# Kernel optimization log

Hardware: AMD Instinct MI355X
Metric: run time of the kernel (lower is better)

The kernel has to match this reference:

```python
import jax, jax.numpy as jnp
import numpy as np

L = 4096   # num_tokens (one prefill sequence)
D = 2048   # hidden_size
HK = 16    # num_k_heads
HV = 32    # num_v_heads
DK = 128   # head_k_dim
DV = 128   # head_v_dim
RATIO = HV // HK
EPS = 1e-6


def setup_inputs() -> dict:
    key = jax.random.key(0)
    ks = jax.random.split(key, 11)
    s = 0.02
    return {
        "hidden_states": jax.random.normal(ks[0], (L, D), jnp.float32),
        "Wq": jax.random.normal(ks[1], (D, HK * DK), jnp.float32) * s,
        "Wk": jax.random.normal(ks[2], (D, HK * DK), jnp.float32) * s,
        "Wv": jax.random.normal(ks[3], (D, HV * DV), jnp.float32) * s,
        "Wz": jax.random.normal(ks[4], (D, HV * DV), jnp.float32) * s,
        "Wb": jax.random.normal(ks[5], (D, HV), jnp.float32) * s,
        "Wa": jax.random.normal(ks[6], (D, HV), jnp.float32) * s,
        "A_log": jnp.log(jax.random.uniform(ks[7], (HV,), jnp.float32, 1.0, 16.0)),
        "dt_bias": jax.random.normal(ks[8], (HV,), jnp.float32) * 0.5,
        "norm_weight": jnp.ones((DV,), jnp.float32),
        "W_out": jax.random.normal(ks[9], (HV * DV, D), jnp.float32) * s,
    }


def _l2norm(x):
    return x * jax.lax.rsqrt(jnp.sum(x * x, axis=-1, keepdims=True) + EPS)


def reference(hidden_states, Wq, Wk, Wv, Wz, Wb, Wa, A_log, dt_bias, norm_weight, W_out):
    h = hidden_states
    # --- input projections (qkvz + ba split) ---
    q = _l2norm((h @ Wq).reshape(L, HK, DK))            # [L, HK, DK]
    k = _l2norm((h @ Wk).reshape(L, HK, DK))
    v = (h @ Wv).reshape(L, HV, DV)                     # [L, HV, DV]
    z = (h @ Wz).reshape(L, HV, DV)                     # gate for RMSNorm
    beta = jax.nn.sigmoid(h @ Wb)                       # [L, HV]
    g = -jnp.exp(A_log) * jax.nn.softplus(h @ Wa + dt_bias)  # [L, HV]
    decay = jnp.exp(g)                                  # per-token per-head decay
    # repeat shared q/k heads to value heads (GQA ratio)
    q = jnp.repeat(q, RATIO, axis=1) * (DK ** -0.5)     # [L, HV, DK]
    k = jnp.repeat(k, RATIO, axis=1)

    # --- gated delta rule recurrence over tokens ---
    def step(S, xs):
        q_t, k_t, v_t, b_t, d_t = xs                    # [HV,DK],[HV,DK],[HV,DV],[HV],[HV]
        S = S * d_t[:, None, None]                      # decay state [HV, DK, DV]
        pred = jnp.einsum('hk,hkv->hv', k_t, S)         # memory readout
        delta = (v_t - pred) * b_t[:, None]             # delta-rule correction
        S = S + k_t[:, :, None] * delta[:, None, :]
        o = jnp.einsum('hk,hkv->hv', q_t, S)
        return S, o

    S0 = jnp.zeros((HV, DK, DV), jnp.float32)
    _, core = jax.lax.scan(step, S0, (q, k, v, beta, decay))  # core: [L, HV, DV]

    # --- gated RMSNorm: x * silu(z), rms-normalize over head dim ---
    x = core * jax.nn.silu(z)
    x = x * jax.lax.rsqrt(jnp.mean(x * x, axis=-1, keepdims=True) + EPS) * norm_weight

    # --- output projection ---
    return x.reshape(L, HV * DV) @ W_out                # [L, D]
```

## Files before the change

### kernel.cpp

```cpp
#include <hip/hip_runtime.h>

#define LTOK 4096
#define DHID 2048
#define HKN  16
#define HVN  32
#define DKK  128
#define NTOT 12288

typedef unsigned short u16;
typedef __attribute__((ext_vector_type(8))) short short8;
typedef __attribute__((ext_vector_type(8))) unsigned short u16x8;
typedef __attribute__((ext_vector_type(4))) unsigned short u16x4;
typedef __attribute__((ext_vector_type(4))) float f32x4;

__device__ __forceinline__ float b2f(u16 u) {
  unsigned int x = ((unsigned int)u) << 16;
  return __builtin_bit_cast(float, x);
}
__device__ __forceinline__ u16 f2bf(float f) {
  unsigned int u = __builtin_bit_cast(unsigned int, f);
  u += 0x7FFFu + ((u >> 16) & 1u);
  return (u16)(u >> 16);
}

template<int C> __device__ __forceinline__ float dppmv(float x) {
  int i = __builtin_amdgcn_update_dpp(0, __builtin_bit_cast(int, x), C, 0xF, 0xF, true);
  return __builtin_bit_cast(float, i);
}
__device__ __forceinline__ float red16(float x) {
  x += dppmv<0xB1>(x);
  x += dppmv<0x4E>(x);
  x += dppmv<0x124>(x);
  x += dppmv<0x128>(x);
  return x;
}

__device__ __forceinline__ void gld16(const void* g, void* l) {
  __builtin_amdgcn_global_load_lds((const __attribute__((address_space(1))) void*)g,
                                   (__attribute__((address_space(3))) void*)l, 16, 0, 0);
}

template<int OFF> __device__ __forceinline__ short8 dsr(unsigned a) {
  short8 r;
  asm volatile("ds_read_b128 %0, %1 offset:%2" : "=v"(r) : "v"(a), "n"(OFF));
  return r;
}

__device__ __forceinline__ int sw16(int r, int c, int rowc) { return (r * rowc + c) ^ ((r & 7) << 3); }

__device__ __forceinline__ void cstore(u16* C, size_t i, float v) { C[i] = f2bf(v); }
__device__ __forceinline__ void cstore(float* C, size_t i, float v) { C[i] = v; }

__global__ __launch_bounds__(256)
void k_cvt(const float* __restrict__ s, u16* __restrict__ d, int n) {
  const int i = (blockIdx.x * 256 + threadIdx.x) * 4;
  const float4 v = *(const float4*)(s + i);
  ushort4 o;
  o.x = f2bf(v.x); o.y = f2bf(v.y); o.z = f2bf(v.z); o.w = f2bf(v.w);
  *(ushort4*)(d + i) = o;
}

__global__ __launch_bounds__(256)
void k_tr(const float* __restrict__ src, u16* __restrict__ dst, int R, int C) {
  __shared__ float tl[32][33];
  const int r0 = blockIdx.y * 32, c0 = blockIdx.x * 32;
  const int tr = threadIdx.x >> 3, tc = (threadIdx.x & 7) * 4;
  const float4 v = *(const float4*)(src + (size_t)(r0 + tr) * C + c0 + tc);
  tl[tr][tc] = v.x; tl[tr][tc + 1] = v.y; tl[tr][tc + 2] = v.z; tl[tr][tc + 3] = v.w;
  __syncthreads();
  ushort4 o;
  o.x = f2bf(tl[tc + 0][tr]); o.y = f2bf(tl[tc + 1][tr]);
  o.z = f2bf(tl[tc + 2][tr]); o.w = f2bf(tl[tc + 3][tr]);
  *(ushort4*)(dst + (size_t)(c0 + tr) * R + r0 + tc) = o;
}

#define MFMA16(a, b, c) __builtin_amdgcn_mfma_f32_16x16x32_bf16(a, b, c, 0, 0, 0)

template<typename OutT, int NWN>
__global__ __launch_bounds__(512, 2)
void k_g256(const u16* __restrict__ A, const u16* __restrict__ Bt, OutT* __restrict__ C,
            int M, int N, int K, int NT) {
  constexpr int BUFE = 8192 + NWN * 2048;
  constexpr int BN = NWN * 64;
  __shared__ u16 Lds[4 * BUFE];
  const int tid = threadIdx.x;
  const int lane = tid & 63, w = tid >> 6;
  const int fr = lane & 15, fq = lane >> 4;
  const int wm = (w >> 2) * 128, wn = (w & 3) * (NWN * 16);
  const int nkt = K >> 5;
  const size_t sK = (size_t)K;

  const int MT = gridDim.x / NT;
  const int nts = (NT < 16) ? NT : 16;
  const int per_super = MT * nts;
  const int super = blockIdx.x / per_super;
  const int within = blockIdx.x % per_super;
  const int mtg = MT >> 3;
  const int q = within >> 3;
  const int mt = (within & 7) * mtg + (q % mtg);
  const int nt = super * nts + q / mtg;

  const int kslot = ((tid & 3) ^ ((tid >> 3) & 3)) * 8;
  const u16* aS = A + (size_t)(mt * 256 + (tid >> 2)) * sK + kslot;
  const u16* bS = Bt + (size_t)(nt * BN + (tid >> 2)) * sK + kslot;

  f32x4 acc[8][NWN] = {};

  auto STAGE = [&](int kt_) {
    const int sk = (kt_ < nkt) ? kt_ : nkt - 1;
    u16* base = &Lds[(kt_ & 3) * BUFE];
    gld16(aS + (size_t)sk * 32, base + w * 512);
    gld16(aS + 128 * sK + (size_t)sk * 32, base + w * 512 + 4096);
    gld16(bS + (size_t)sk * 32, base + 8192 + w * 512);
    if constexpr (NWN == 4)
      gld16(bS + 128 * sK + (size_t)sk * 32, base + 8192 + w * 512 + 4096);
  };

  STAGE(0); STAGE(1); STAGE(2);

  const int akey = (fr >> 1) & 3;
  const unsigned ldsBase = (unsigned)(size_t)(__attribute__((address_space(3))) void*)&Lds[0];
  const unsigned aA0 = ldsBase + 2u * (unsigned)((wm + fr) * 32 + ((fq ^ akey) << 3));
  const unsigned bA0 = ldsBase + 2u * (unsigned)(8192 + (wn + fr) * 32 + ((fq ^ akey) << 3));

  for (int kt = 0; kt < nkt; ++kt) {
    if constexpr (NWN == 4) asm volatile("s_waitcnt vmcnt(8)" ::: "memory");
    else                    asm volatile("s_waitcnt vmcnt(6)" ::: "memory");
    __builtin_amdgcn_s_barrier();
    __builtin_amdgcn_sched_barrier(0);
    STAGE(kt + 3);
    const unsigned bo = (unsigned)((kt & 3) * BUFE * 2);
    const unsigned aA = aA0 + bo, bA = bA0 + bo;
    short8 af[8], bf[NWN];
    bf[0] = dsr<0>(bA); bf[1] = dsr<1024>(bA);
    if constexpr (NWN == 4) { bf[2] = dsr<2048>(bA); bf[3] = dsr<3072>(bA); }
    af[0] = dsr<0>(aA);    af[1] = dsr<1024>(aA);
    af[2] = dsr<2048>(aA); af[3] = dsr<3072>(aA);
    af[4] = dsr<4096>(aA); af[5] = dsr<5120>(aA);
    af[6] = dsr<6144>(aA); af[7] = dsr<7168>(aA);
    asm volatile("s_waitcnt lgkmcnt(6)" ::: "memory");
    __builtin_amdgcn_sched_barrier(0);
    __builtin_amdgcn_s_setprio(1);
#pragma unroll
    for (int j = 0; j < NWN; ++j) { acc[0][j] = MFMA16(af[0], bf[j], acc[0][j]);
                                    acc[1][j] = MFMA16(af[1], bf[j], acc[1][j]); }
    asm volatile("s_waitcnt lgkmcnt(4)" ::: "memory");
    __builtin_amdgcn_sched_barrier(0);
#pragma unroll
    for (int j = 0; j < NWN; ++j) { acc[2][j] = MFMA16(af[2], bf[j], acc[2][j]);
                                    acc[3][j] = MFMA16(af[3], bf[j], acc[3][j]); }
    asm volatile("s_waitcnt lgkmcnt(2)" ::: "memory");
    __builtin_amdgcn_sched_barrier(0);
#pragma unroll
    for (int j = 0; j < NWN; ++j) { acc[4][j] = MFMA16(af[4], bf[j], acc[4][j]);
                                    acc[5][j] = MFMA16(af[5], bf[j], acc[5][j]); }
    asm volatile("s_waitcnt lgkmcnt(0)" ::: "memory");
    __builtin_amdgcn_sched_barrier(0);
#pragma unroll
    for (int j = 0; j < NWN; ++j) { acc[6][j] = MFMA16(af[6], bf[j], acc[6][j]);
                                    acc[7][j] = MFMA16(af[7], bf[j], acc[7][j]); }
    __builtin_amdgcn_s_setprio(0);
  }

  const int r0 = mt * 256 + wm + fq * 4;
  const int c0 = nt * BN + wn + fr;
#pragma unroll
  for (int i = 0; i < 8; ++i)
#pragma unroll
    for (int j = 0; j < NWN; ++j)
#pragma unroll
      for (int e = 0; e < 4; ++e)
        cstore(C, (size_t)(r0 + i * 16 + e) * N + c0 + j * 16, acc[i][j][e]);
}

__global__ __launch_bounds__(256)
void k_ba(const float* __restrict__ h, const float* __restrict__ Wb, const float* __restrict__ Wa,
          const float* __restrict__ A_log, const float* __restrict__ dtb,
          float* __restrict__ beta, float* __restrict__ g_out) {
  const int w = threadIdx.x >> 6, lane = threadIdx.x & 63;
  const int t = blockIdx.x * 4 + w;
  const int j = lane & 31;
  const bool isB = lane < 32;
  const float* __restrict__ hr = h + (size_t)t * DHID;
  const float* Wc = isB ? Wb : Wa;
  float acc = 0.f;
  for (int kk = 0; kk < DHID; ++kk) acc = fmaf(hr[kk], Wc[(size_t)kk * HVN + j], acc);
  if (isB) {
    beta[(size_t)t * HVN + j] = 1.f / (1.f + expf(-acc));
  } else {
    float xx = acc + dtb[j];
    float sp = (xx > 20.f) ? xx : log1pf(expf(xx));
    g_out[(size_t)t * HVN + j] = -expf(A_log[j]) * sp;
  }
}

__global__ __launch_bounds__(256)
void k_l2n(u16* __restrict__ qkvz) {
  const int w = threadIdx.x >> 6, lane = threadIdx.x & 63;
  const int r = blockIdx.x * 4 + w;
  const int isK = r >> 16;
  const int rr = r & 65535;
  const int t = rr >> 4, hd = rr & 15;
  u16* p = qkvz + (size_t)t * NTOT + isK * 2048 + hd * DKK + lane * 2;
  float a = b2f(p[0]), b = b2f(p[1]);
  float ss = a * a + b * b;
  ss = red16(ss);
  ss += __shfl_xor(ss, 16);
  ss += __shfl_xor(ss, 32);
  const float sc = rsqrtf(ss + 1e-6f) * (isK ? 1.f : 0.08838834764831845f);
  p[0] = f2bf(a * sc); p[1] = f2bf(b * sc);
}

__global__ __launch_bounds__(256)
void k_r1(const u16* __restrict__ qkvz, const float* __restrict__ beta_g,
          const float* __restrict__ g_g, u16* __restrict__ UM_g, float* __restrict__ cumL_g) {
  const int pair = blockIdx.x;
  const int hv = pair >> 6, n = pair & 63;
  const int hk = hv >> 1;
  const int t0 = n * 64;
  const int tid = threadIdx.x, lane = tid & 63, wv = tid >> 6;
  const int fr = lane & 15, fq = lane >> 4;

  __shared__ __align__(16) u16 Xb[256 * 64];
  __shared__ __align__(16) u16 Dbuf0[64 * 64 * 2];
  __shared__ __align__(16) u16 Dbuf1[64 * 64 * 2];
  __shared__ float Lc[64];
  __shared__ float Bc[64];
  u16* Kl = Dbuf0;

  const int j = tid & 63, h = tid >> 6;
  const u16* kg = qkvz + (size_t)(t0 + j) * NTOT + 2048 + hk * DKK + h * 32;
  const u16* vg = qkvz + (size_t)(t0 + j) * NTOT + 4096 + hv * DKK + h * 32;
  u16x8 kv[4], vv[4];
#pragma unroll
  for (int i = 0; i < 4; ++i) { kv[i] = *(const u16x8*)(kg + i * 8); vv[i] = *(const u16x8*)(vg + i * 8); }
  if (tid < 64) {
    Lc[tid] = g_g[(size_t)(t0 + tid) * HVN + hv];
    Bc[tid] = beta_g[(size_t)(t0 + tid) * HVN + hv];
  }
#pragma unroll
  for (int i = 0; i < 4; ++i) *(u16x8*)&Kl[sw16(j, h * 32 + i * 8, 128)] = kv[i];
  __syncthreads();
  if (tid == 0) { float a = 0.f; for (int t = 0; t < 64; ++t) { a += Lc[t]; Lc[t] = a; } }
  __syncthreads();
  if (tid < 64) cumL_g[(size_t)pair * 64 + tid] = Lc[tid];

  {
    const float bj = Bc[j];
    const float mj = bj * __expf(Lc[j]);
#pragma unroll
    for (int i = 0; i < 4; ++i)
#pragma unroll
      for (int e = 0; e < 8; ++e) {
        int c = h * 32 + i * 8 + e;
        Xb[sw16(c, j, 64)] = f2bf(bj * b2f(vv[i][e]));
        Xb[sw16(128 + c, j, 64)] = f2bf(mj * b2f(kv[i][e]));
      }
  }
  f32x4 kk[4] = {};
#pragma unroll
  for (int ks = 0; ks < 4; ++ks) {
    short8 afr = *(const short8*)&Kl[sw16(wv * 16 + fr, ks * 32 + fq * 8, 128)];
#pragma unroll
    for (int ct = 0; ct < 4; ++ct) {
      short8 bfr = *(const short8*)&Kl[sw16(ct * 16 + fr, ks * 32 + fq * 8, 128)];
      kk[ct] = MFMA16(afr, bfr, kk[ct]);
    }
  }
  __syncthreads();

  f32x4 acc[16];
#pragma unroll
  for (int ct = 0; ct < 16; ++ct) {
    u16x4 xi = *(const u16x4*)&Xb[sw16(ct * 16 + fr, wv * 16 + fq * 4, 64)];
    acc[ct][0] = b2f(xi[0]); acc[ct][1] = b2f(xi[1]); acc[ct][2] = b2f(xi[2]); acc[ct][3] = b2f(xi[3]);
  }
#pragma unroll
  for (int ct = 0; ct < 4; ++ct) {
    const int s = ct * 16 + fr;
    u16x4 pk;
#pragma unroll
    for (int e = 0; e < 4; ++e) {
      const int t = wv * 16 + fq * 4 + e;
      float v = (s < t) ? -Bc[t] * __expf(Lc[t] - Lc[s]) * kk[ct][e] : 0.f;
      pk[e] = f2bf(v);
      Dbuf0[sw16(t, s, 64)] = pk[e];
    }
    *(u16x4*)&Dbuf0[4096 + sw16(s, wv * 16 + fq * 4, 64)] = pk;
  }
  __syncthreads();

  u16* DA = Dbuf0;
  u16* DB = Dbuf1;
  for (int stg = 0; stg < 6; ++stg) {
    u16* Dr = DA;
    u16* Dc = DA + 4096;
    short8 da0 = *(const short8*)&Dr[sw16(wv * 16 + fr, 0 + fq * 8, 64)];
    short8 da1 = *(const short8*)&Dr[sw16(wv * 16 + fr, 32 + fq * 8, 64)];
#pragma unroll
    for (int ct = 0; ct < 16; ++ct) {
      short8 b0 = *(const short8*)&Xb[sw16(ct * 16 + fr, 0 + fq * 8, 64)];
      short8 b1 = *(const short8*)&Xb[sw16(ct * 16 + fr, 32 + fq * 8, 64)];
      acc[ct] = MFMA16(da0, b0, acc[ct]);
      acc[ct] = MFMA16(da1, b1, acc[ct]);
    }
    f32x4 sq[4] = {};
    if (stg < 5) {
#pragma unroll
      for (int ct = 0; ct < 4; ++ct) {
        short8 sb0 = *(const short8*)&Dc[sw16(ct * 16 + fr, 0 + fq * 8, 64)];
        short8 sb1 = *(const short8*)&Dc[sw16(ct * 16 + fr, 32 + fq * 8, 64)];
        sq[ct] = MFMA16(da0, sb0, sq[ct]);
        sq[ct] = MFMA16(da1, sb1, sq[ct]);
      }
    }
    __syncthreads();
#pragma unroll
    for (int ct = 0; ct < 16; ++ct) {
      u16x4 pk;
      pk[0] = f2bf(acc[ct][0]); pk[1] = f2bf(acc[ct][1]); pk[2] = f2bf(acc[ct][2]); pk[3] = f2bf(acc[ct][3]);
      *(u16x4*)&Xb[sw16(ct * 16 + fr, wv * 16 + fq * 4, 64)] = pk;
    }
    if (stg < 5) {
#pragma unroll
      for (int ct = 0; ct < 4; ++ct) {
        u16x4 pk;
        pk[0] = f2bf(sq[ct][0]); pk[1] = f2bf(sq[ct][1]); pk[2] = f2bf(sq[ct][2]); pk[3] = f2bf(sq[ct][3]);
        *(u16x4*)&(DB + 4096)[sw16(ct * 16 + fr, wv * 16 + fq * 4, 64)] = pk;
#pragma unroll
        for (int e = 0; e < 4; ++e) DB[sw16(wv * 16 + fq * 4 + e, ct * 16 + fr, 64)] = pk[e];
      }
    }
    __syncthreads();
    u16* tmp = DA; DA = DB; DB = tmp;
  }

#pragma unroll
  for (int ct = 0; ct < 16; ++ct) {
    const int c = ct * 16 + fr;
#pragma unroll
    for (int e = 0; e < 4; ++e) {
      const int t = wv * 16 + fq * 4 + e;
      float v = acc[ct][e];
      if (ct >= 8) v = -v;
      UM_g[((size_t)pair * 64 + t) * 256 + c] = f2bf(v);
    }
  }
}

__global__ __launch_bounds__(512)
void k_r2(u16* __restrict__ qkvz, const u16* __restrict__ UM_g,
          const float* __restrict__ cumL_g, u16* __restrict__ o1_g) {
  const int hv = blockIdx.x >> 2, cs = blockIdx.x & 3;
  const int hk = hv >> 1;
  const int tid = threadIdx.x, lane = tid & 63, w = tid >> 6;
  const int fr = lane & 15, fq = lane >> 4;
  const int j = tid & 63, h = tid >> 6;
  const int tw = w & 3, dwv = w >> 2;

  __shared__ __align__(16) u16 Ml2[2][8192];
  __shared__ __align__(16) u16 Ql2[2][8192];
  __shared__ __align__(16) u16 Kt2[2][8192];
  __shared__ __align__(16) u16 dT[2048];
  __shared__ __align__(16) u16 SbT[4096];
  __shared__ __align__(16) u16 o1b[2048];
  __shared__ float Lc2[2][64];

  f32x4 sacc[2];
#pragma unroll
  for (int d = 0; d < 2; ++d) sacc[d] = (f32x4){0.f, 0.f, 0.f, 0.f};
  for (int i = tid; i < 4096; i += 512) SbT[i] = 0;

  u16x8 pQ0, pQ1, pK0, pK1, pM0, pM1;
  u16 pUn0, pUn1, pUn2, pUn3, pUc0, pUc1, pUc2, pUc3;
  float pL, pL63;

#define PREF(nn) {                                                            \
    const int nc = ((nn) < 64) ? (nn) : 63;                                   \
    const int pr = hv * 64 + nc; const int tt0 = nc * 64;                     \
    const u16* qg = qkvz + (size_t)(tt0 + j) * NTOT + hk * DKK + h * 16;      \
    pQ0 = *(const u16x8*)qg;          pQ1 = *(const u16x8*)(qg + 8);          \
    pK0 = *(const u16x8*)(qg + 2048); pK1 = *(const u16x8*)(qg + 2056);       \
    const u16* mg = UM_g + ((size_t)pr * 64 + j) * 256;                       \
    pM0 = *(const u16x8*)(mg + 128 + h * 16);                                 \
    pM1 = *(const u16x8*)(mg + 136 + h * 16);                                 \
    const u16* ug = UM_g + ((size_t)pr * 64 + tw * 16 + fq * 4) * 256         \
                    + cs * 32 + dwv * 16 + fr;                                \
    pUn0 = ug[0]; pUn1 = ug[256]; pUn2 = ug[512]; pUn3 = ug[768];             \
    pL = cumL_g[(size_t)pr * 64 + j]; pL63 = cumL_g[(size_t)pr * 64 + 63]; }

#define STW(b) {                                                              \
    *(u16x8*)&Ql2[b][sw16(j, h * 16, 128)] = pQ0;                             \
    *(u16x8*)&Ql2[b][sw16(j, h * 16 + 8, 128)] = pQ1;                         \
    *(u16x8*)&Ml2[b][sw16(j, h * 16, 128)] = pM0;                             \
    *(u16x8*)&Ml2[b][sw16(j, h * 16 + 8, 128)] = pM1;                         \
    const float scK = __expf(pL63 - pL);                                      \
    _Pragma("unroll")                                                         \
    for (int e = 0; e < 8; ++e) {                                             \
      Kt2[b][sw16(h * 16 + e, j, 64)] = f2bf(scK * b2f(pK0[e]));              \
      Kt2[b][sw16(h * 16 + 8 + e, j, 64)] = f2bf(scK * b2f(pK1[e]));          \
    }                                                                         \
    if (h == 0) Lc2[b][j] = pL; }

  PREF(0)
  STW(0)
  __syncthreads();

  for (int n = 0; n < 64; ++n) {
    const int cur = n & 1;
    const int pair = hv * 64 + n, t0 = n * 64;
    pUc0 = pUn0; pUc1 = pUn1; pUc2 = pUn2; pUc3 = pUn3;
    const float curL63 = pL63;
    PREF(n + 1)

    short8 amf[4], aqf[4];
#pragma unroll
    for (int ks = 0; ks < 4; ++ks) {
      amf[ks] = *(const short8*)&Ml2[cur][sw16(tw * 16 + fr, ks * 32 + fq * 8, 128)];
      aqf[ks] = *(const short8*)&Ql2[cur][sw16(tw * 16 + fr, ks * 32 + fq * 8, 128)];
    }
    float el[4];
#pragma unroll
    for (int e = 0; e < 4; ++e) el[e] = __expf(Lc2[cur][tw * 16 + fq * 4 + e]);
    {
      f32x4 dc;
      dc[0] = b2f(pUc0); dc[1] = b2f(pUc1); dc[2] = b2f(pUc2); dc[3] = b2f(pUc3);
      f32x4 oc = {};
#pragma unroll
      for (int ks = 0; ks < 4; ++ks) {
        short8 bs = *(const short8*)&SbT[sw16(dwv * 16 + fr, ks * 32 + fq * 8, 128)];
        dc = MFMA16(amf[ks], bs, dc);
        oc = MFMA16(aqf[ks], bs, oc);
      }
      u16x4 pkd;
      pkd[0] = f2bf(dc[0]); pkd[1] = f2bf(dc[1]); pkd[2] = f2bf(dc[2]); pkd[3] = f2bf(dc[3]);
      *(u16x4*)&dT[sw16(dwv * 16 + fr, tw * 16 + fq * 4, 64)] = pkd;
      u16x4 pko;
#pragma unroll
      for (int e = 0; e < 4; ++e) pko[e] = f2bf(oc[e] * el[e]);
      *(u16x4*)&o1b[sw16(dwv * 16 + fr, tw * 16 + fq * 4, 64)] = pko;
    }
    __syncthreads();

    {
      const int i = tid * 4;
      u16x4 vd = *(const u16x4*)&dT[i];
      const int f = cs * 2048 + i;
      *(u16x4*)(qkvz + (size_t)(t0 + (f >> 7)) * NTOT + 4096 + hv * DKK + (f & 127)) = vd;
      u16x4 vo = *(const u16x4*)&o1b[i];
      *(u16x4*)(o1_g + (size_t)pair * 8192 + cs * 2048 + i) = vo;
    }
    STW(cur ^ 1)
    {
      const float eC = __expf(curL63);
      short8 ak0 = *(const short8*)&Kt2[cur][sw16(w * 16 + fr, fq * 8, 64)];
      short8 ak1 = *(const short8*)&Kt2[cur][sw16(w * 16 + fr, 32 + fq * 8, 64)];
#pragma unroll
      for (int d = 0; d < 2; ++d) {
        short8 bd0 = *(const short8*)&dT[sw16(d * 16 + fr, fq * 8, 64)];
        short8 bd1 = *(const short8*)&dT[sw16(d * 16 + fr, 32 + fq * 8, 64)];
        f32x4 sa = sacc[d];
#pragma unroll
        for (int e = 0; e < 4; ++e) sa[e] *= eC;
        sa = MFMA16(ak0, bd0, sa);
        sa = MFMA16(ak1, bd1, sa);
        sacc[d] = sa;
        u16x4 pk;
        pk[0] = f2bf(sa[0]); pk[1] = f2bf(sa[1]); pk[2] = f2bf(sa[2]); pk[3] = f2bf(sa[3]);
        *(u16x4*)&SbT[sw16(d * 16 + fr, w * 16 + fq * 4, 128)] = pk;
      }
    }
    __syncthreads();
  }
#undef PREF
#undef STW
}

__global__ __launch_bounds__(512)
void k_r3(const u16* __restrict__ qkvz, const u16* __restrict__ o1_g,
          const float* __restrict__ cumL_g, const float* __restrict__ nw,
          u16* __restrict__ x) {
  const int pair = blockIdx.x, hv = pair >> 6, n = pair & 63, hk = hv >> 1, t0 = n * 64;
  const int tid = threadIdx.x, lane = tid & 63, w = tid >> 6;
  const int fr = lane & 15, fq = lane >> 4;
  const int j = tid & 63, h = tid >> 6;

  __shared__ __align__(16) u16 Ql[8192];
  __shared__ __align__(16) u16 Kl[8192];
  __shared__ __align__(16) u16 Gl[4096];
  __shared__ __align__(16) u16 dTl[8192];
  __shared__ __align__(16) u16 o1l[8192];
  __shared__ __align__(16) float of[64 * 132];
  __shared__ float Lc[64];
  __shared__ float Lw[128];

  {
    const u16* qg = qkvz + (size_t)(t0 + j) * NTOT + hk * DKK + h * 16;
    u16x8 q0 = *(const u16x8*)qg, q1 = *(const u16x8*)(qg + 8);
    u16x8 k0 = *(const u16x8*)(qg + 2048), k1 = *(const u16x8*)(qg + 2056);
    *(u16x8*)&Ql[sw16(j, h * 16, 128)] = q0;
    *(u16x8*)&Ql[sw16(j, h * 16 + 8, 128)] = q1;
    *(u16x8*)&Kl[sw16(j, h * 16, 128)] = k0;
    *(u16x8*)&Kl[sw16(j, h * 16 + 8, 128)] = k1;
  }
#pragma unroll
  for (int it = 0; it < 2; ++it) {
    const int f = ((w * 2 + it) * 64 + lane) * 8;
    gld16(qkvz + (size_t)(t0 + (f >> 7)) * NTOT + 4096 + hv * DKK + (f & 127),
          (char*)dTl + (w * 2 + it) * 1024);
    gld16(o1_g + (size_t)pair * 8192 + f, (char*)o1l + (w * 2 + it) * 1024);
  }
  if (tid < 64) Lc[tid] = cumL_g[(size_t)pair * 64 + tid];
  if (tid < 128) Lw[tid] = nw[tid];
  __syncthreads();

  const int tw = w & 3, sp = (w >> 2) * 2;
  {
    f32x4 kk0 = {}, kk1 = {};
#pragma unroll
    for (int ks = 0; ks < 4; ++ks) {
      short8 aq = *(const short8*)&Ql[sw16(tw * 16 + fr, ks * 32 + fq * 8, 128)];
      short8 b0 = *(const short8*)&Kl[sw16(sp * 16 + fr, ks * 32 + fq * 8, 128)];
      short8 b1 = *(const short8*)&Kl[sw16((sp + 1) * 16 + fr, ks * 32 + fq * 8, 128)];
      kk0 = MFMA16(aq, b0, kk0);
      kk1 = MFMA16(aq, b1, kk1);
    }
#pragma unroll
    for (int e = 0; e < 4; ++e) {
      const int t = tw * 16 + fq * 4 + e;
      const float Lt = Lc[t];
      const int s0 = sp * 16 + fr, s1 = s0 + 16;
      Gl[sw16(t, s0, 64)] = f2bf((s0 <= t) ? kk0[e] * __expf(Lt - Lc[s0]) : 0.f);
      Gl[sw16(t, s1, 64)] = f2bf((s1 <= t) ? kk1[e] * __expf(Lt - Lc[s1]) : 0.f);
    }
  }
  __syncthreads();

  {
    short8 ag0 = *(const short8*)&Gl[sw16(tw * 16 + fr, fq * 8, 64)];
    short8 ag1 = *(const short8*)&Gl[sw16(tw * 16 + fr, 32 + fq * 8, 64)];
#pragma unroll
    for (int dd = 0; dd < 4; ++dd) {
      const int d = (w >> 2) * 4 + dd;
      short8 bd0 = *(const short8*)&dTl[sw16(d * 16 + fr, fq * 8, 64)];
      short8 bd1 = *(const short8*)&dTl[sw16(d * 16 + fr, 32 + fq * 8, 64)];
      f32x4 oc = {};
      oc = MFMA16(ag0, bd0, oc);
      oc = MFMA16(ag1, bd1, oc);
#pragma unroll
      for (int e = 0; e < 4; ++e) of[(tw * 16 + fq * 4 + e) * 132 + d * 16 + fr] = oc[e];
    }
  }
  __syncthreads();

  {
    const int t = tid >> 3, q8 = tid & 7;
    const u16* zp = qkvz + (size_t)(t0 + t) * NTOT + 8192 + hv * DKK + q8 * 16;
    float xv[16];
    float ss = 0.f;
#pragma unroll
    for (int i = 0; i < 2; ++i) {
      u16x8 zv = *(const u16x8*)(zp + i * 8);
#pragma unroll
      for (int e = 0; e < 8; ++e) {
        const int dv = q8 * 16 + i * 8 + e;
        float z = b2f(zv[e]);
        float o = of[t * 132 + dv] + b2f(o1l[sw16(dv, t, 64)]);
        float xx = o * (z / (1.f + __expf(-z)));
        xv[i * 8 + e] = xx;
        ss = fmaf(xx, xx, ss);
      }
    }
    ss += __shfl_xor(ss, 1);
    ss += __shfl_xor(ss, 2);
    ss += __shfl_xor(ss, 4);
    const float scl = rsqrtf(ss * (1.f / 128.f) + 1e-6f);
    u16* xo = x + (size_t)(t0 + t) * 4096 + hv * DKK + q8 * 16;
#pragma unroll
    for (int i = 0; i < 2; ++i) {
      u16x8 pk;
#pragma unroll
      for (int e = 0; e < 8; ++e) pk[e] = f2bf(xv[i * 8 + e] * scl * Lw[q8 * 16 + i * 8 + e]);
      *(u16x8*)(xo + i * 8) = pk;
    }
  }
}

extern "C" void kernel_launch(void* const* d_in, const int* in_sizes, int n_in,
                              void* d_out, int out_size, void* d_ws, size_t ws_size,
                              hipStream_t stream) {
  const float* h    = (const float*)d_in[0];
  const float* Wq   = (const float*)d_in[1];
  const float* Wk   = (const float*)d_in[2];
  const float* Wv   = (const float*)d_in[3];
  const float* Wz   = (const float*)d_in[4];
  const float* Wb   = (const float*)d_in[5];
  const float* Wa   = (const float*)d_in[6];
  const float* Alog = (const float*)d_in[7];
  const float* dtb  = (const float*)d_in[8];
  const float* nw   = (const float*)d_in[9];
  const float* Wo   = (const float*)d_in[10];
  char* ws = (char*)d_ws;
  u16* h_bf  = (u16*)(ws);
  u16* Wt    = (u16*)(ws + 16777216ull);
  u16* UM    = (u16*)(ws);
  u16* Wto   = (u16*)(ws + 67108864ull);
  u16* qkvz  = (u16*)(ws + 83886080ull);
  u16* o1g   = (u16*)(ws + 184549376ull);
  u16* xbuf  = (u16*)(ws + 16777216ull);
  float* beta  = (float*)(ws + 218103808ull);
  float* g     = (float*)(ws + 218103808ull + 524288ull);
  float* cumL  = (float*)(ws + 218103808ull + 1048576ull);

  k_cvt<<<8192, 256, 0, stream>>>(h, h_bf, LTOK * DHID);
  k_tr<<<dim3(64, 64), 256, 0, stream>>>(Wq, Wt, 2048, 2048);
  k_tr<<<dim3(64, 64), 256, 0, stream>>>(Wk, Wt + 2048ull * 2048, 2048, 2048);
  k_tr<<<dim3(128, 64), 256, 0, stream>>>(Wv, Wt + 4096ull * 2048, 2048, 4096);
  k_tr<<<dim3(128, 64), 256, 0, stream>>>(Wz, Wt + 8192ull * 2048, 2048, 4096);
  k_tr<<<dim3(64, 128), 256, 0, stream>>>(Wo, Wto, 4096, 2048);
  k_g256<u16, 4><<<768, 512, 0, stream>>>(h_bf, Wt, qkvz, 4096, 12288, 2048, 48);
  k_ba<<<1024, 256, 0, stream>>>(h, Wb, Wa, Alog, dtb, beta, g);
  k_l2n<<<32768, 256, 0, stream>>>(qkvz);
  k_r1<<<2048, 256, 0, stream>>>(qkvz, beta, g, UM, cumL);
  k_r2<<<128, 512, 0, stream>>>(qkvz, UM, cumL, o1g);
  k_r3<<<2048, 512, 0, stream>>>(qkvz, o1g, cumL, nw, xbuf);
  k_g256<float, 2><<<256, 512, 0, stream>>>(xbuf, Wto, (float*)d_out, 4096, 2048, 4096, 16);
}
```

Baseline: 812.4 us.

## Double-buffer GEMM LDS fragments in registers to overlap reads with MFMA

The GEMM main loop now keeps two sets of A/B register fragments and is unrolled by two. While the MFMAs for the current k-tile run, the LDS reads for the next k-tile are issued. The global prefetch for tile kt+3 is also moved ahead of the vmcnt wait and the barrier. This is meant to hide LDS read latency behind matrix work instead of stalling on staged lgkmcnt waits. In exchange it doubles fragment register use, which may reduce occupancy, and it assumes an even tile count.

```diff
diff --git a/kernel.cpp b/kernel.cpp
--- a/kernel.cpp
+++ b/kernel.cpp
@@ -123,44 +123,49 @@
   const unsigned aA0 = ldsBase + 2u * (unsigned)((wm + fr) * 32 + ((fq ^ akey) << 3));
   const unsigned bA0 = ldsBase + 2u * (unsigned)(8192 + (wn + fr) * 32 + ((fq ^ akey) << 3));
 
-  for (int kt = 0; kt < nkt; ++kt) {
-    if constexpr (NWN == 4) asm volatile("s_waitcnt vmcnt(8)" ::: "memory");
-    else                    asm volatile("s_waitcnt vmcnt(6)" ::: "memory");
-    __builtin_amdgcn_s_barrier();
-    __builtin_amdgcn_sched_barrier(0);
-    STAGE(kt + 3);
-    const unsigned bo = (unsigned)((kt & 3) * BUFE * 2);
-    const unsigned aA = aA0 + bo, bA = bA0 + bo;
-    short8 af[8], bf[NWN];
-    bf[0] = dsr<0>(bA); bf[1] = dsr<1024>(bA);
-    if constexpr (NWN == 4) { bf[2] = dsr<2048>(bA); bf[3] = dsr<3072>(bA); }
-    af[0] = dsr<0>(aA);    af[1] = dsr<1024>(aA);
-    af[2] = dsr<2048>(aA); af[3] = dsr<3072>(aA);
-    af[4] = dsr<4096>(aA); af[5] = dsr<5120>(aA);
-    af[6] = dsr<6144>(aA); af[7] = dsr<7168>(aA);
-    asm volatile("s_waitcnt lgkmcnt(6)" ::: "memory");
-    __builtin_amdgcn_sched_barrier(0);
-    __builtin_amdgcn_s_setprio(1);
-#pragma unroll
-    for (int j = 0; j < NWN; ++j) { acc[0][j] = MFMA16(af[0], bf[j], acc[0][j]);
-                                    acc[1][j] = MFMA16(af[1], bf[j], acc[1][j]); }
-    asm volatile("s_waitcnt lgkmcnt(4)" ::: "memory");
-    __builtin_amdgcn_sched_barrier(0);
-#pragma unroll
-    for (int j = 0; j < NWN; ++j) { acc[2][j] = MFMA16(af[2], bf[j], acc[2][j]);
-                                    acc[3][j] = MFMA16(af[3], bf[j], acc[3][j]); }
-    asm volatile("s_waitcnt lgkmcnt(2)" ::: "memory");
-    __builtin_amdgcn_sched_barrier(0);
-#pragma unroll
-    for (int j = 0; j < NWN; ++j) { acc[4][j] = MFMA16(af[4], bf[j], acc[4][j]);
-                                    acc[5][j] = MFMA16(af[5], bf[j], acc[5][j]); }
-    asm volatile("s_waitcnt lgkmcnt(0)" ::: "memory");
-    __builtin_amdgcn_sched_barrier(0);
-#pragma unroll
-    for (int j = 0; j < NWN; ++j) { acc[6][j] = MFMA16(af[6], bf[j], acc[6][j]);
-                                    acc[7][j] = MFMA16(af[7], bf[j], acc[7][j]); }
-    __builtin_amdgcn_s_setprio(0);
-  }
+  short8 afA[8], bfA[NWN], afB[8], bfB[NWN];
+
+#define RD(afX, bfX, kt_) {                                                   \
+    const unsigned bo = (unsigned)(((kt_) & 3) * BUFE * 2);                   \
+    const unsigned aAr = aA0 + bo, bAr = bA0 + bo;                            \
+    bfX[0] = dsr<0>(bAr); bfX[1] = dsr<1024>(bAr);                            \
+    if constexpr (NWN == 4) { bfX[2] = dsr<2048>(bAr); bfX[3] = dsr<3072>(bAr); } \
+    afX[0] = dsr<0>(aAr);    afX[1] = dsr<1024>(aAr);                         \
+    afX[2] = dsr<2048>(aAr); afX[3] = dsr<3072>(aAr);                         \
+    afX[4] = dsr<4096>(aAr); afX[5] = dsr<5120>(aAr);                         \
+    afX[6] = dsr<6144>(aAr); afX[7] = dsr<7168>(aAr); }
+
+  if constexpr (NWN == 4) asm volatile("s_waitcnt vmcnt(8)" ::: "memory");
+  else                    asm volatile("s_waitcnt vmcnt(6)" ::: "memory");
+  __builtin_amdgcn_s_barrier();
+  RD(afA, bfA, 0)
+  asm volatile("s_waitcnt lgkmcnt(0)" ::: "memory");
+  __builtin_amdgcn_sched_barrier(0);
+
+#define ITER(kt_, afC, bfC, afN, bfN) {                                       \
+    STAGE((kt_) + 3);                                                         \
+    if constexpr (NWN == 4) asm volatile("s_waitcnt vmcnt(8)" ::: "memory");  \
+    else                    asm volatile("s_waitcnt vmcnt(6)" ::: "memory");  \
+    __builtin_amdgcn_s_barrier();                                             \
+    __builtin_amdgcn_sched_barrier(0);                                        \
+    RD(afN, bfN, (kt_) + 1)                                                   \
+    __builtin_amdgcn_sched_barrier(0);                                        \
+    __builtin_amdgcn_s_setprio(1);                                            \
+    _Pragma("unroll")                                                         \
+    for (int i = 0; i < 8; ++i)                                               \
+      _Pragma("unroll")                                                       \
+      for (int j = 0; j < NWN; ++j)                                           \
+        acc[i][j] = MFMA16(afC[i], bfC[j], acc[i][j]);                        \
+    __builtin_amdgcn_s_setprio(0);                                            \
+    asm volatile("s_waitcnt lgkmcnt(0)" ::: "memory");                        \
+    __builtin_amdgcn_sched_barrier(0); }
+
+  for (int kt = 0; kt < nkt; kt += 2) {
+    ITER(kt, afA, bfA, afB, bfB)
+    ITER(kt + 1, afB, bfB, afA, bfA)
+  }
+#undef ITER
+#undef RD
 
   const int r0 = mt * 256 + wm + fq * 4;
   const int c0 = nt * BN + wn + fr;
```

Result: no change. 818.0 us (+0.7%).
